# Performance work log

Hardware: AMD Instinct MI355X
Metric: run time of the kernel (lower is better)

The kernel has to match this reference:

```python
import jax, jax.numpy as jnp
import numpy as np

H = 16  # num_heads (matches init_kwargs)
MASK_VAL = -10000.0


def setup_inputs() -> dict:
    key = jax.random.key(0)
    k1, k2, k3, k4, k5 = jax.random.split(key, 5)
    B, N, C = 2, 2048, 1024
    hidden_states = jax.random.normal(k1, (B, N, C), dtype=jnp.float32)
    encoder_hidden_states = jax.random.normal(k2, (B, N, C), dtype=jnp.float32)
    pad_mask = jax.random.bernoulli(k3, 0.1, (B, N))
    # Linear weights stored as (in, out); scaled ~Xavier so softmax isn't saturated
    W_q = jax.random.normal(k4, (C, C), dtype=jnp.float32) * (C ** -0.5)
    W_c = jax.random.normal(k5, (C, 2 * C), dtype=jnp.float32) * (C ** -0.5)
    return {"hidden_states": hidden_states,
            "encoder_hidden_states": encoder_hidden_states,
            "pad_mask": pad_mask,
            "W_q": W_q,
            "W_c": W_c}


def _split_heads(x, B, N, C):
    # (B, N, C) -> (B, H, N, D)
    return x.reshape(B, N, H, C // H).transpose(0, 2, 1, 3)


def reference(hidden_states, encoder_hidden_states, pad_mask, W_q, W_c):
    B, N, C = hidden_states.shape
    D = C // H
    scaler = D ** -0.5

    q = hidden_states @ W_q                       # (B, N, C)
    kv = encoder_hidden_states @ W_c              # (B, N, 2C)
    k, v = kv[..., :C], kv[..., C:]

    q = _split_heads(q, B, N, C)                  # (B, H, N, D)
    k = _split_heads(k, B, N, C)
    v = _split_heads(v, B, N, C)

    scores = jnp.einsum('bhid,bhjd->bhij', q, k) * scaler  # (B, H, N, N)

    # construct_mask: expanded[b,i,j] = pad_mask[b,i] OR pad_mask[b,j]
    expanded = pad_mask[:, None, :, None] | pad_mask[:, None, None, :]
    scores = jnp.where(expanded, MASK_VAL, scores)

    # max-subtract + softmax (dropout_rate=0 so dropout is identity)
    scores = scores - jax.lax.stop_gradient(scores.max(axis=-1, keepdims=True))
    att_weights = jax.nn.softmax(scores, axis=-1)

    att = jnp.einsum('bhij,bhjd->bhid', att_weights, v)   # (B, H, N, D)
    att = att.transpose(0, 2, 1, 3).reshape(B, N, C)
    return att, att_weights
```

## Files before the change

### kernel.cpp

```cpp
#include <hip/hip_runtime.h>
#include <math.h>

#define B_ 2
#define N_ 2048
#define C_ 1024
#define H_ 16
#define D_ 64

typedef __attribute__((ext_vector_type(8))) short short8v;
typedef __attribute__((ext_vector_type(4))) short short4v;
typedef __attribute__((ext_vector_type(4))) float f32x4;

static __device__ __forceinline__ short f2bf(float f) {
    union { float f; unsigned u; } v; v.f = f;
    unsigned r = v.u + 0x7FFFu + ((v.u >> 16) & 1u);
    return (short)(r >> 16);
}

static __device__ __forceinline__ void splitbf(float f, short& h, short& l) {
    union { float f; unsigned u; } v; v.f = f;
    const unsigned uh = v.u & 0xFFFF0000u;
    h = (short)(uh >> 16);
    union { unsigned u; float f; } w; w.u = uh;
    union { float f; unsigned u; } x; x.f = f - w.f;
    l = (short)(x.u >> 16);
}

__global__ __launch_bounds__(256) void split_a(const float* __restrict__ src,
                                               short* __restrict__ hi,
                                               short* __restrict__ lo) {
    const int i = (blockIdx.x * 256 + threadIdx.x) * 4;
    const float4 f = *(const float4*)&src[i];
    short4v h, l;
    short th_, tl_;
    splitbf(f.x, th_, tl_); h[0] = th_; l[0] = tl_;
    splitbf(f.y, th_, tl_); h[1] = th_; l[1] = tl_;
    splitbf(f.z, th_, tl_); h[2] = th_; l[2] = tl_;
    splitbf(f.w, th_, tl_); h[3] = th_; l[3] = tl_;
    *(short4v*)&hi[i] = h;
    *(short4v*)&lo[i] = l;
}

__global__ __launch_bounds__(256) void split_wt(const float* __restrict__ Wm,
                                                short* __restrict__ th,
                                                short* __restrict__ tl,
                                                int K, int N) {
    __shared__ float Ls[64][68];
    const int t  = threadIdx.x;
    const int n0 = blockIdx.x * 64;
    const int k0 = blockIdx.y * 64;
#pragma unroll
    for (int it = 0; it < 4; ++it) {
        const int kl = it * 16 + (t >> 4);
        const int nl = (t & 15) * 4;
        *(float4*)&Ls[kl][nl] = *(const float4*)&Wm[(size_t)(k0 + kl) * N + n0 + nl];
    }
    __syncthreads();
#pragma unroll
    for (int it = 0; it < 4; ++it) {
        const int idx = it * 256 + t;
        const int nl  = idx & 63;
        const int ks  = (idx >> 6) * 4;
        short4v h, l;
#pragma unroll
        for (int j = 0; j < 4; ++j) {
            short th_, tl_;
            splitbf(Ls[ks + j][nl], th_, tl_);
            h[j] = th_; l[j] = tl_;
        }
        *(short4v*)&th[(size_t)(n0 + nl) * K + k0 + ks] = h;
        *(short4v*)&tl[(size_t)(n0 + nl) * K + k0 + ks] = l;
    }
}

#define GKSTR 40

__global__ __launch_bounds__(256) void gemm_bf3(const short* __restrict__ Ah,
                                                const short* __restrict__ Al,
                                                const short* __restrict__ Bth,
                                                const short* __restrict__ Btl,
                                                short* __restrict__ Cm,
                                                int K, int N) {
    __shared__ __align__(16) short Ahs[128][GKSTR];
    __shared__ __align__(16) short Als[128][GKSTR];
    __shared__ __align__(16) short Bhs[128][GKSTR];
    __shared__ __align__(16) short Bls[128][GKSTR];

    const int t  = threadIdx.x;
    const int w  = t >> 6;
    const int lq = t & 15;
    const int hq = (t & 63) >> 4;
    const int wr = w >> 1;
    const int wc = w & 1;
    const int m0 = blockIdx.y * 128;
    const int n0 = blockIdx.x * 128;

    const int srow = t >> 1;
    const int scol = (t & 1) * 16;

    const short* gA_h = &Ah[(size_t)(m0 + srow) * K + scol];
    const short* gA_l = &Al[(size_t)(m0 + srow) * K + scol];
    const short* gB_h = &Bth[(size_t)(n0 + srow) * K + scol];
    const short* gB_l = &Btl[(size_t)(n0 + srow) * K + scol];

    f32x4 acc[4][4];
#pragma unroll
    for (int mi = 0; mi < 4; ++mi)
#pragma unroll
        for (int ni = 0; ni < 4; ++ni) acc[mi][ni] = (f32x4){0.f, 0.f, 0.f, 0.f};

    short8v ra_h0 = *(const short8v*)gA_h,       ra_h1 = *(const short8v*)(gA_h + 8);
    short8v ra_l0 = *(const short8v*)gA_l,       ra_l1 = *(const short8v*)(gA_l + 8);
    short8v rb_h0 = *(const short8v*)gB_h,       rb_h1 = *(const short8v*)(gB_h + 8);
    short8v rb_l0 = *(const short8v*)gB_l,       rb_l1 = *(const short8v*)(gB_l + 8);

    for (int k0 = 0; k0 < K; k0 += 32) {
        __syncthreads();
        *(short8v*)&Ahs[srow][scol]     = ra_h0;
        *(short8v*)&Ahs[srow][scol + 8] = ra_h1;
        *(short8v*)&Als[srow][scol]     = ra_l0;
        *(short8v*)&Als[srow][scol + 8] = ra_l1;
        *(short8v*)&Bhs[srow][scol]     = rb_h0;
        *(short8v*)&Bhs[srow][scol + 8] = rb_h1;
        *(short8v*)&Bls[srow][scol]     = rb_l0;
        *(short8v*)&Bls[srow][scol + 8] = rb_l1;
        __syncthreads();

        const int kn = k0 + 32;
        if (kn < K) {
            ra_h0 = *(const short8v*)(gA_h + kn); ra_h1 = *(const short8v*)(gA_h + kn + 8);
            ra_l0 = *(const short8v*)(gA_l + kn); ra_l1 = *(const short8v*)(gA_l + kn + 8);
            rb_h0 = *(const short8v*)(gB_h + kn); rb_h1 = *(const short8v*)(gB_h + kn + 8);
            rb_l0 = *(const short8v*)(gB_l + kn); rb_l1 = *(const short8v*)(gB_l + kn + 8);
        }

        short8v bnh[4], bnl[4];
#pragma unroll
        for (int ni = 0; ni < 4; ++ni) {
            bnh[ni] = *(const short8v*)&Bhs[wc * 64 + ni * 16 + lq][hq * 8];
            bnl[ni] = *(const short8v*)&Bls[wc * 64 + ni * 16 + lq][hq * 8];
        }
#pragma unroll
        for (int mi = 0; mi < 4; ++mi) {
            const short8v amh = *(const short8v*)&Ahs[wr * 64 + mi * 16 + lq][hq * 8];
            const short8v aml = *(const short8v*)&Als[wr * 64 + mi * 16 + lq][hq * 8];
#pragma unroll
            for (int ni = 0; ni < 4; ++ni) {
                acc[mi][ni] = __builtin_amdgcn_mfma_f32_16x16x32_bf16(amh, bnh[ni], acc[mi][ni], 0, 0, 0);
                acc[mi][ni] = __builtin_amdgcn_mfma_f32_16x16x32_bf16(amh, bnl[ni], acc[mi][ni], 0, 0, 0);
                acc[mi][ni] = __builtin_amdgcn_mfma_f32_16x16x32_bf16(aml, bnh[ni], acc[mi][ni], 0, 0, 0);
            }
        }
    }

#pragma unroll
    for (int mi = 0; mi < 4; ++mi)
#pragma unroll
        for (int ni = 0; ni < 4; ++ni) {
            const int col = n0 + wc * 64 + ni * 16 + lq;
#pragma unroll
            for (int r = 0; r < 4; ++r) {
                const int row = m0 + wr * 64 + mi * 16 + hq * 4 + r;
                Cm[(size_t)row * N + col] = f2bf(acc[mi][ni][r]);
            }
        }
}

__global__ __launch_bounds__(256) void v_transpose(const short* __restrict__ kv_bf,
                                                   short* __restrict__ vt) {
    __shared__ __align__(16) short Ls[128][72];
    const int t  = threadIdx.x;
    const int jt = blockIdx.x * 128;
    const int h  = blockIdx.y;
    const int b  = blockIdx.z;
    const short* src = kv_bf + (size_t)b * N_ * 2 * C_ + C_ + h * D_;
#pragma unroll
    for (int it = 0; it < 4; ++it) {
        const int idx = it * 256 + t;
        const int j = idx >> 3, d0 = (idx & 7) * 8;
        *(short8v*)&Ls[j][d0] = *(const short8v*)&src[(size_t)(jt + j) * (2 * C_) + d0];
    }
    __syncthreads();
    short* dst = vt + ((size_t)(b * H_ + h)) * D_ * N_;
#pragma unroll
    for (int it = 0; it < 4; ++it) {
        const int idx = it * 256 + t;
        const int d  = idx >> 4;
        const int j0 = (idx & 15) * 8;
        short8v s;
#pragma unroll
        for (int jj = 0; jj < 8; ++jj) s[jj] = Ls[j0 + jj][d];
        *(short8v*)&dst[(size_t)d * N_ + jt + j0] = s;
    }
}

#define KSTR 72
#define VSTR 136
#define PSTR 136

__global__ __launch_bounds__(256) void attn_mfma(const short* __restrict__ q,
                                                 const short* __restrict__ kv,
                                                 const short* __restrict__ vtg,
                                                 const int* __restrict__ mask,
                                                 float* __restrict__ out_att,
                                                 float* __restrict__ out_w) {
    __shared__ __align__(16) short Ks[128][KSTR];
    __shared__ __align__(16) short Vt[64][VSTR];
    __shared__ __align__(16) short Ps[4][32][PSTR];
    __shared__ float linv_s[4][32];
    __shared__ int   mcol_s[128];

    const int t  = threadIdx.x;
    const int w  = t >> 6;
    const int l  = t & 63;
    const int lq = l & 15;
    const int hq = l >> 4;

    const int lin = blockIdx.x;
    const int swz = (lin & 7) * 64 + (lin >> 3);
    const int qb = swz & 15;
    const int h  = (swz >> 4) & 15;
    const int b  = swz >> 8;
    const int i0 = qb * 128 + w * 32;

    const int sj = t >> 3;
    const int sd = (t & 7) * 8;
    const int vd = t >> 4;
    const int vj = (t & 15) * 8;

    short8v qa[2][2];
#pragma unroll
    for (int g = 0; g < 2; ++g) {
        const short* qrow = q + ((size_t)(b * N_ + i0 + g * 16 + lq)) * C_ + h * D_;
        qa[g][0] = *(const short8v*)&qrow[hq * 8];
        qa[g][1] = *(const short8v*)&qrow[32 + hq * 8];
    }

    int mr[2][4];
#pragma unroll
    for (int g = 0; g < 2; ++g)
#pragma unroll
        for (int r = 0; r < 4; ++r) mr[g][r] = mask[b * N_ + i0 + g * 16 + hq * 4 + r];

    const short* kbase = kv + (size_t)b * N_ * 2 * C_ + h * D_;
    const short* vtb   = vtg + ((size_t)(b * H_ + h)) * D_ * N_;

    float lsum[2][4];
#pragma unroll
    for (int g = 0; g < 2; ++g)
#pragma unroll
        for (int r = 0; r < 4; ++r) lsum[g][r] = 0.f;

    short8v kr[4];
    int mpre = 0;
#pragma unroll
    for (int it = 0; it < 4; ++it)
        kr[it] = *(const short8v*)&kbase[(size_t)(it * 32 + sj) * (2 * C_) + sd];
    if (t < 128) mpre = mask[b * N_ + t];

    for (int tile = 0; tile < 16; ++tile) {
        __syncthreads();
#pragma unroll
        for (int it = 0; it < 4; ++it)
            *(short8v*)&Ks[it * 32 + sj][sd] = kr[it];
        if (t < 128) mcol_s[t] = mpre;
        __syncthreads();

        if (tile < 15) {
            const int jn = (tile + 1) * 128;
#pragma unroll
            for (int it = 0; it < 4; ++it)
                kr[it] = *(const short8v*)&kbase[(size_t)(jn + it * 32 + sj) * (2 * C_) + sd];
            if (t < 128) mpre = mask[b * N_ + jn + t];
        }

#pragma unroll
        for (int cb = 0; cb < 8; ++cb) {
            const short8v b0 = *(short8v*)&Ks[cb * 16 + lq][hq * 8];
            const short8v b1 = *(short8v*)&Ks[cb * 16 + lq][32 + hq * 8];
            const int mc = mcol_s[cb * 16 + lq];
#pragma unroll
            for (int g = 0; g < 2; ++g) {
                f32x4 acc = {0.f, 0.f, 0.f, 0.f};
                acc = __builtin_amdgcn_mfma_f32_16x16x32_bf16(qa[g][0], b0, acc, 0, 0, 0);
                acc = __builtin_amdgcn_mfma_f32_16x16x32_bf16(qa[g][1], b1, acc, 0, 0, 0);
#pragma unroll
                for (int r = 0; r < 4; ++r)
                    lsum[g][r] += mr[g][r] ? 1.0f : (mc ? 0.0f : __expf(acc[r] * 0.125f));
            }
        }
    }
    float inv[2][4];
#pragma unroll
    for (int g = 0; g < 2; ++g)
#pragma unroll
        for (int r = 0; r < 4; ++r) {
            float s = lsum[g][r];
#pragma unroll
            for (int off = 1; off < 16; off <<= 1) s += __shfl_xor(s, off, 64);
            inv[g][r] = 1.0f / s;
        }
    if (lq == 0)
#pragma unroll
        for (int g = 0; g < 2; ++g)
#pragma unroll
            for (int r = 0; r < 4; ++r) linv_s[w][g * 16 + hq * 4 + r] = inv[g][r];

    float* wbase[2];
#pragma unroll
    for (int g = 0; g < 2; ++g)
        wbase[g] = out_w + ((size_t)((b * H_ + h) * N_ + i0 + g * 16 + hq * 4)) * N_;

    f32x4 oacc[4][2];
#pragma unroll
    for (int db = 0; db < 4; ++db)
#pragma unroll
        for (int g = 0; g < 2; ++g) oacc[db][g] = (f32x4){0.f, 0.f, 0.f, 0.f};

    short8v vr[4];
#pragma unroll
    for (int it = 0; it < 4; ++it) {
        kr[it] = *(const short8v*)&kbase[(size_t)(it * 32 + sj) * (2 * C_) + sd];
        vr[it] = *(const short8v*)&vtb[(size_t)(it * 16 + vd) * N_ + vj];
    }
    if (t < 128) mpre = mask[b * N_ + t];

    for (int tile = 0; tile < 16; ++tile) {
        const int jt = tile * 128;
        __syncthreads();
#pragma unroll
        for (int it = 0; it < 4; ++it) {
            *(short8v*)&Ks[it * 32 + sj][sd] = kr[it];
            *(short8v*)&Vt[it * 16 + vd][vj] = vr[it];
        }
        if (t < 128) mcol_s[t] = mpre;
        __syncthreads();

        if (tile < 15) {
            const int jn = jt + 128;
#pragma unroll
            for (int it = 0; it < 4; ++it) {
                kr[it] = *(const short8v*)&kbase[(size_t)(jn + it * 32 + sj) * (2 * C_) + sd];
                vr[it] = *(const short8v*)&vtb[(size_t)(it * 16 + vd) * N_ + jn + vj];
            }
            if (t < 128) mpre = mask[b * N_ + jn + t];
        }

#pragma unroll
        for (int cb = 0; cb < 8; ++cb) {
            const short8v b0 = *(short8v*)&Ks[cb * 16 + lq][hq * 8];
            const short8v b1 = *(short8v*)&Ks[cb * 16 + lq][32 + hq * 8];
            const int mc   = mcol_s[cb * 16 + lq];
            const int jcol = cb * 16 + lq;
#pragma unroll
            for (int g = 0; g < 2; ++g) {
                f32x4 acc = {0.f, 0.f, 0.f, 0.f};
                acc = __builtin_amdgcn_mfma_f32_16x16x32_bf16(qa[g][0], b0, acc, 0, 0, 0);
                acc = __builtin_amdgcn_mfma_f32_16x16x32_bf16(qa[g][1], b1, acc, 0, 0, 0);
#pragma unroll
                for (int r = 0; r < 4; ++r) {
                    const float ev = mr[g][r] ? 1.0f : (mc ? 0.0f : __expf(acc[r] * 0.125f));
                    wbase[g][(size_t)r * N_ + jt + jcol] = ev * inv[g][r];
                    Ps[w][g * 16 + hq * 4 + r][jcol] = f2bf(ev);
                }
            }
        }
        __syncthreads();

        short8v pb[2][4];
#pragma unroll
        for (int kb = 0; kb < 4; ++kb) {
            pb[0][kb] = *(short8v*)&Ps[w][lq][kb * 32 + hq * 8];
            pb[1][kb] = *(short8v*)&Ps[w][16 + lq][kb * 32 + hq * 8];
        }
#pragma unroll
        for (int db = 0; db < 4; ++db)
#pragma unroll
            for (int kb = 0; kb < 4; ++kb) {
                const short8v va = *(short8v*)&Vt[db * 16 + lq][kb * 32 + hq * 8];
                oacc[db][0] = __builtin_amdgcn_mfma_f32_16x16x32_bf16(va, pb[0][kb], oacc[db][0], 0, 0, 0);
                oacc[db][1] = __builtin_amdgcn_mfma_f32_16x16x32_bf16(va, pb[1][kb], oacc[db][1], 0, 0, 0);
            }
    }

#pragma unroll
    for (int g = 0; g < 2; ++g) {
        const float invi = linv_s[w][g * 16 + lq];
        const size_t abase = ((size_t)(b * N_ + i0 + g * 16 + lq)) * C_ + h * D_;
#pragma unroll
        for (int db = 0; db < 4; ++db)
#pragma unroll
            for (int r = 0; r < 4; ++r)
                out_att[abase + db * 16 + hq * 4 + r] = oacc[db][g][r] * invi;
    }
}

extern "C" void kernel_launch(void* const* d_in, const int* in_sizes, int n_in,
                              void* d_out, int out_size, void* d_ws, size_t ws_size,
                              hipStream_t stream) {
    const float* hs   = (const float*)d_in[0];
    const float* ehs  = (const float*)d_in[1];
    const int*   mask = (const int*)d_in[2];
    const float* W_q  = (const float*)d_in[3];
    const float* W_c  = (const float*)d_in[4];

    float* out_att = (float*)d_out;
    float* out_w   = (float*)d_out + (size_t)B_ * N_ * C_;

    const size_t M1 = (size_t)1024 * 1024;
    short* qbf  = (short*)d_ws;
    short* kvbf = qbf + 4 * M1;
    short* Ah   = kvbf + 8 * M1;
    short* Al   = Ah + 4 * M1;
    short* vt   = Ah;
    short* Wth  = Al + 4 * M1;
    short* Wtl  = Wth + 2 * M1;

    const int nelems_a = B_ * N_ * C_;

    split_a<<<dim3(nelems_a / 1024), 256, 0, stream>>>(hs, Ah, Al);
    split_wt<<<dim3(C_ / 64, C_ / 64), 256, 0, stream>>>(W_q, Wth, Wtl, C_, C_);
    gemm_bf3<<<dim3(C_ / 128, (B_ * N_) / 128), 256, 0, stream>>>(
        Ah, Al, Wth, Wtl, qbf, C_, C_);

    split_a<<<dim3(nelems_a / 1024), 256, 0, stream>>>(ehs, Ah, Al);
    split_wt<<<dim3((2 * C_) / 64, C_ / 64), 256, 0, stream>>>(W_c, Wth, Wtl, C_, 2 * C_);
    gemm_bf3<<<dim3((2 * C_) / 128, (B_ * N_) / 128), 256, 0, stream>>>(
        Ah, Al, Wth, Wtl, kvbf, C_, 2 * C_);

    v_transpose<<<dim3(N_ / 128, H_, B_), 256, 0, stream>>>(kvbf, vt);
    attn_mfma<<<dim3(512), 256, 0, stream>>>(
        qbf, kvbf, vt, mask, out_att, out_w);
}
```

Measured before the change: 324.4 us.

## Read K, V and mask directly from global memory, dropping LDS staging

```diff
diff --git a/kernel.cpp b/kernel.cpp
--- a/kernel.cpp
+++ b/kernel.cpp
@@ -194,8 +194,6 @@
     }
 }
 
-#define KSTR 72
-#define VSTR 136
 #define PSTR 136
 
 __global__ __launch_bounds__(256) void attn_mfma(const short* __restrict__ q,
@@ -204,11 +202,8 @@
                                                  const int* __restrict__ mask,
                                                  float* __restrict__ out_att,
                                                  float* __restrict__ out_w) {
-    __shared__ __align__(16) short Ks[128][KSTR];
-    __shared__ __align__(16) short Vt[64][VSTR];
     __shared__ __align__(16) short Ps[4][32][PSTR];
     __shared__ float linv_s[4][32];
-    __shared__ int   mcol_s[128];
 
     const int t  = threadIdx.x;
     const int w  = t >> 6;
@@ -223,11 +218,6 @@
     const int b  = swz >> 8;
     const int i0 = qb * 128 + w * 32;
 
-    const int sj = t >> 3;
-    const int sd = (t & 7) * 8;
-    const int vd = t >> 4;
-    const int vj = (t & 15) * 8;
-
     short8v qa[2][2];
 #pragma unroll
     for (int g = 0; g < 2; ++g) {
@@ -244,6 +234,7 @@
 
     const short* kbase = kv + (size_t)b * N_ * 2 * C_ + h * D_;
     const short* vtb   = vtg + ((size_t)(b * H_ + h)) * D_ * N_;
+    const int*   mbase = mask + b * N_;
 
     float lsum[2][4];
 #pragma unroll
@@ -251,43 +242,20 @@
 #pragma unroll
         for (int r = 0; r < 4; ++r) lsum[g][r] = 0.f;
 
-    short8v kr[4];
-    int mpre = 0;
-#pragma unroll
-    for (int it = 0; it < 4; ++it)
-        kr[it] = *(const short8v*)&kbase[(size_t)(it * 32 + sj) * (2 * C_) + sd];
-    if (t < 128) mpre = mask[b * N_ + t];
-
-    for (int tile = 0; tile < 16; ++tile) {
-        __syncthreads();
-#pragma unroll
-        for (int it = 0; it < 4; ++it)
-            *(short8v*)&Ks[it * 32 + sj][sd] = kr[it];
-        if (t < 128) mcol_s[t] = mpre;
-        __syncthreads();
-
-        if (tile < 15) {
-            const int jn = (tile + 1) * 128;
-#pragma unroll
-            for (int it = 0; it < 4; ++it)
-                kr[it] = *(const short8v*)&kbase[(size_t)(jn + it * 32 + sj) * (2 * C_) + sd];
-            if (t < 128) mpre = mask[b * N_ + jn + t];
-        }
-
-#pragma unroll
-        for (int cb = 0; cb < 8; ++cb) {
-            const short8v b0 = *(short8v*)&Ks[cb * 16 + lq][hq * 8];
-            const short8v b1 = *(short8v*)&Ks[cb * 16 + lq][32 + hq * 8];
-            const int mc = mcol_s[cb * 16 + lq];
-#pragma unroll
-            for (int g = 0; g < 2; ++g) {
-                f32x4 acc = {0.f, 0.f, 0.f, 0.f};
-                acc = __builtin_amdgcn_mfma_f32_16x16x32_bf16(qa[g][0], b0, acc, 0, 0, 0);
-                acc = __builtin_amdgcn_mfma_f32_16x16x32_bf16(qa[g][1], b1, acc, 0, 0, 0);
-#pragma unroll
-                for (int r = 0; r < 4; ++r)
-                    lsum[g][r] += mr[g][r] ? 1.0f : (mc ? 0.0f : __expf(acc[r] * 0.125f));
-            }
+    for (int cb0 = 0; cb0 < 128; ++cb0) {
+        const int j = cb0 * 16 + lq;
+        const short* krow = kbase + (size_t)j * (2 * C_);
+        const short8v b0 = *(const short8v*)&krow[hq * 8];
+        const short8v b1 = *(const short8v*)&krow[32 + hq * 8];
+        const int mc = mbase[j];
+#pragma unroll
+        for (int g = 0; g < 2; ++g) {
+            f32x4 acc = {0.f, 0.f, 0.f, 0.f};
+            acc = __builtin_amdgcn_mfma_f32_16x16x32_bf16(qa[g][0], b0, acc, 0, 0, 0);
+            acc = __builtin_amdgcn_mfma_f32_16x16x32_bf16(qa[g][1], b1, acc, 0, 0, 0);
+#pragma unroll
+            for (int r = 0; r < 4; ++r)
+                lsum[g][r] += mr[g][r] ? 1.0f : (mc ? 0.0f : __expf(acc[r] * 0.125f));
         }
     }
     float inv[2][4];
@@ -317,41 +285,16 @@
 #pragma unroll
         for (int g = 0; g < 2; ++g) oacc[db][g] = (f32x4){0.f, 0.f, 0.f, 0.f};
 
-    short8v vr[4];
-#pragma unroll
-    for (int it = 0; it < 4; ++it) {
-        kr[it] = *(const short8v*)&kbase[(size_t)(it * 32 + sj) * (2 * C_) + sd];
-        vr[it] = *(const short8v*)&vtb[(size_t)(it * 16 + vd) * N_ + vj];
-    }
-    if (t < 128) mpre = mask[b * N_ + t];
-
     for (int tile = 0; tile < 16; ++tile) {
         const int jt = tile * 128;
-        __syncthreads();
-#pragma unroll
-        for (int it = 0; it < 4; ++it) {
-            *(short8v*)&Ks[it * 32 + sj][sd] = kr[it];
-            *(short8v*)&Vt[it * 16 + vd][vj] = vr[it];
-        }
-        if (t < 128) mcol_s[t] = mpre;
-        __syncthreads();
-
-        if (tile < 15) {
-            const int jn = jt + 128;
-#pragma unroll
-            for (int it = 0; it < 4; ++it) {
-                kr[it] = *(const short8v*)&kbase[(size_t)(jn + it * 32 + sj) * (2 * C_) + sd];
-                vr[it] = *(const short8v*)&vtb[(size_t)(it * 16 + vd) * N_ + jn + vj];
-            }
-            if (t < 128) mpre = mask[b * N_ + jn + t];
-        }
 
 #pragma unroll
         for (int cb = 0; cb < 8; ++cb) {
-            const short8v b0 = *(short8v*)&Ks[cb * 16 + lq][hq * 8];
-            const short8v b1 = *(short8v*)&Ks[cb * 16 + lq][32 + hq * 8];
-            const int mc   = mcol_s[cb * 16 + lq];
             const int jcol = cb * 16 + lq;
+            const short* krow = kbase + (size_t)(jt + jcol) * (2 * C_);
+            const short8v b0 = *(const short8v*)&krow[hq * 8];
+            const short8v b1 = *(const short8v*)&krow[32 + hq * 8];
+            const int mc = mbase[jt + jcol];
 #pragma unroll
             for (int g = 0; g < 2; ++g) {
                 f32x4 acc = {0.f, 0.f, 0.f, 0.f};
@@ -365,7 +308,6 @@
                 }
             }
         }
-        __syncthreads();
 
         short8v pb[2][4];
 #pragma unroll
@@ -377,7 +319,7 @@
         for (int db = 0; db < 4; ++db)
 #pragma unroll
             for (int kb = 0; kb < 4; ++kb) {
-                const short8v va = *(short8v*)&Vt[db * 16 + lq][kb * 32 + hq * 8];
+                const short8v va = *(const short8v*)&vtb[(size_t)(db * 16 + lq) * N_ + jt + kb * 32 + hq * 8];
                 oacc[db][0] = __builtin_amdgcn_mfma_f32_16x16x32_bf16(va, pb[0][kb], oacc[db][0], 0, 0, 0);
                 oacc[db][1] = __builtin_amdgcn_mfma_f32_16x16x32_bf16(va, pb[1][kb], oacc[db][1], 0, 0, 0);
             }
```

Result: slower. 523.9 us (+61.5%).
